# Optimization experiments

Hardware: AMD Instinct MI355X
Metric: run time of the kernel (lower is better)

## Reference

```python
import jax, jax.numpy as jnp
import numpy as np

N_NODES = 500_000
N_EDGES = 16_000_000


def setup_inputs() -> dict:
    key = jax.random.key(0)
    ks = jax.random.split(key, 8)
    x = jax.random.normal(ks[0], (N_NODES, 6), dtype=jnp.float32)
    edge_index = jax.random.randint(ks[1], (2, N_EDGES), 0, N_NODES, dtype=jnp.int64)
    conv_w = jax.random.normal(ks[2], (4, 6), dtype=jnp.float32) * 0.4
    conv_b = jax.random.normal(ks[3], (4,), dtype=jnp.float32) * 0.1
    fc1_w = jax.random.normal(ks[4], (64, 4), dtype=jnp.float32) * 0.5
    fc1_b = jax.random.normal(ks[5], (64,), dtype=jnp.float32) * 0.1
    fc3_w = jax.random.normal(ks[6], (10, 64), dtype=jnp.float32) * 0.125
    fc3_b = jax.random.normal(ks[7], (10,), dtype=jnp.float32) * 0.1
    return {"x": x, "edge_index": edge_index, "conv_w": conv_w, "conv_b": conv_b,
            "fc1_w": fc1_w, "fc1_b": fc1_b, "fc3_w": fc3_w, "fc3_b": fc3_b}


def reference(x, edge_index, conv_w, conv_b, fc1_w, fc1_b, fc3_w, fc3_b):
    n = x.shape[0]
    loop = jnp.arange(n, dtype=edge_index.dtype)
    # PyG GCNConv default: add self-loops, symmetric normalization
    row = jnp.concatenate([edge_index[0], loop])  # source
    col = jnp.concatenate([edge_index[1], loop])  # target (aggregation index)
    deg = jax.ops.segment_sum(jnp.ones_like(col, dtype=x.dtype), col, num_segments=n)
    dinv = jnp.where(deg > 0, deg ** -0.5, 0.0).astype(x.dtype)
    norm = dinv[row] * dinv[col]                  # [E+N]
    h = x @ conv_w.T                              # [N, 4]
    msg = h[row] * norm[:, None]                  # gather + scale
    agg = jax.ops.segment_sum(msg, col, num_segments=n) + conv_b  # scatter-add
    t = jnp.tanh(agg)
    # F.dropout treated as identity (deterministic eval reference)
    g = jnp.mean(t, axis=0, keepdims=True)        # global_mean_pool, batch=None -> [1, 4]
    hdn = jax.nn.relu(g @ fc1_w.T + fc1_b)
    out = hdn @ fc3_w.T + fc3_b                   # [1, output_size]
    return out
```

## Files before the change

kernel.cpp:

```cpp
#include <hip/hip_runtime.h>
#include <hip/hip_fp16.h>
#include <math.h>


constexpr int NP = 1024;
constexpr int SHIFT = 10;
constexpr unsigned MASK = 1023;
constexpr int NPART_MAX = 512;
constexpr int EPB = 8192;
constexpr int BINB = 512;
constexpr int BT = 512;
constexpr int SPLIT = 4;

struct alignas(8) Half4 { __half2 a, b; };

typedef unsigned u32x4 __attribute__((ext_vector_type(4)));
typedef int      i32x4 __attribute__((ext_vector_type(4)));
typedef float    f32x4 __attribute__((ext_vector_type(4)));


__global__ __launch_bounds__(BINB) void k_bin(const int* __restrict__ row,
                                              const int* __restrict__ col, int E,
                                              int P, int cap, int* __restrict__ cursor,
                                              unsigned* __restrict__ binned) {
    __shared__ unsigned lbuf[EPB];
    __shared__ int lcount[NPART_MAX];
    __shared__ int lbase[NPART_MAX];
    __shared__ int gbase[NPART_MAX];
    __shared__ int lpos[NPART_MAX];
    __shared__ int sc[NPART_MAX];

    int t = threadIdx.x;
    int start = blockIdx.x * EPB;
    int end = min(start + EPB, E);
    bool full = (end - start) == EPB;

    lcount[t] = 0; lpos[t] = 0;
    __syncthreads();

    if (full) {
        const int4* c4 = (const int4*)(col + start);
#pragma unroll
        for (int i = 0; i < EPB / 4 / BINB; ++i) {
            int4 c = c4[t + i * BINB];
            atomicAdd(&lcount[c.x >> SHIFT], 1);
            atomicAdd(&lcount[c.y >> SHIFT], 1);
            atomicAdd(&lcount[c.z >> SHIFT], 1);
            atomicAdd(&lcount[c.w >> SHIFT], 1);
        }
    } else {
        for (int e = start + t; e < end; e += BINB)
            atomicAdd(&lcount[col[e] >> SHIFT], 1);
    }
    __syncthreads();

    sc[t] = lcount[t];
    __syncthreads();
    for (int off = 1; off < NPART_MAX; off <<= 1) {
        int v = (t >= off) ? sc[t - off] : 0;
        __syncthreads();
        sc[t] += v;
        __syncthreads();
    }
    lbase[t] = sc[t] - lcount[t];
    if (t < P) {
        int c = lcount[t];
        gbase[t] = (c > 0) ? atomicAdd(&cursor[t], c) : 0;
    }
    __syncthreads();

    if (full) {
        const int4* c4 = (const int4*)(col + start);
        const i32x4* r4 = (const i32x4*)(row + start);
#pragma unroll
        for (int i = 0; i < EPB / 4 / BINB; ++i) {
            int4 c = c4[t + i * BINB];
            i32x4 r = __builtin_nontemporal_load(&r4[t + i * BINB]);
            int part, slot;
            part = c.x >> SHIFT; slot = atomicAdd(&lpos[part], 1);
            lbuf[lbase[part] + slot] = ((unsigned)r.x << SHIFT) | ((unsigned)c.x & MASK);
            part = c.y >> SHIFT; slot = atomicAdd(&lpos[part], 1);
            lbuf[lbase[part] + slot] = ((unsigned)r.y << SHIFT) | ((unsigned)c.y & MASK);
            part = c.z >> SHIFT; slot = atomicAdd(&lpos[part], 1);
            lbuf[lbase[part] + slot] = ((unsigned)r.z << SHIFT) | ((unsigned)c.z & MASK);
            part = c.w >> SHIFT; slot = atomicAdd(&lpos[part], 1);
            lbuf[lbase[part] + slot] = ((unsigned)r.w << SHIFT) | ((unsigned)c.w & MASK);
        }
    } else {
        for (int e = start + t; e < end; e += BINB) {
            int r = row[e], c = col[e];
            int part = c >> SHIFT;
            int slot = atomicAdd(&lpos[part], 1);
            lbuf[lbase[part] + slot] = ((unsigned)r << SHIFT) | ((unsigned)c & MASK);
        }
    }
    __syncthreads();

    int lane = t & 63;
    int wave = t >> 6;
    const int nwaves = BINB / 64;
    for (int part = wave; part < P; part += nwaves) {
        int cnt = lcount[part];
        if (cnt == 0) continue;
        int lb = lbase[part];
        int gb = gbase[part];
        unsigned* dst = binned + (size_t)part * cap;
        for (int j = lane; j < cnt; j += 64) {
            int slot = gb + j;
            if (slot < cap) __builtin_nontemporal_store(lbuf[lb + j], &dst[slot]);
        }
    }
}

__global__ __launch_bounds__(BT) void k_deg_bin(const unsigned* __restrict__ binned,
                                                const int* __restrict__ cursor, int cap,
                                                int n, int* __restrict__ deg) {
    __shared__ int degs[NP];
    int part = blockIdx.x / SPLIT;
    int sub = blockIdx.x - part * SPLIT;
    int tid = threadIdx.x;
    for (int i = tid; i < NP; i += BT) degs[i] = 0;
    __syncthreads();
    int cnt = min(cursor[part], cap);
    const unsigned* bin = binned + (size_t)part * cap;
    const u32x4* bin4 = (const u32x4*)bin;
    int cnt4 = cnt >> 2;
    for (int i = tid + sub * BT; i < cnt4; i += BT * SPLIT) {
        u32x4 v = __builtin_nontemporal_load(&bin4[i]);
        atomicAdd(&degs[v.x & MASK], 1);
        atomicAdd(&degs[v.y & MASK], 1);
        atomicAdd(&degs[v.z & MASK], 1);
        atomicAdd(&degs[v.w & MASK], 1);
    }
    if (sub == 0) {
        for (int e = (cnt4 << 2) + tid; e < cnt; e += BT)
            atomicAdd(&degs[bin[e] & MASK], 1);
    }
    __syncthreads();
    int base = part * NP;
    for (int i = tid; i < NP; i += BT) {
        int node = base + i;
        if (node < n && degs[i] > 0) atomicAdd(&deg[node], degs[i]);
    }
}

__global__ __launch_bounds__(256) void k_node2(const float* __restrict__ x,
                                               const float* __restrict__ conv_w,
                                               const int* __restrict__ deg, int n,
                                               Half4* __restrict__ ph,
                                               float* __restrict__ dinvg) {
    __shared__ float w[24];
    if (threadIdx.x < 24) w[threadIdx.x] = conv_w[threadIdx.x];
    __syncthreads();
    int i = blockIdx.x * 256 + threadIdx.x;
    if (i >= n) return;
    float dinv = rsqrtf((float)(deg[i] + 1));
    const float* xr = x + (size_t)i * 6;
    float2 a = *(const float2*)xr;
    float2 b = *(const float2*)(xr + 2);
    float2 cc = *(const float2*)(xr + 4);
    float xv[6] = {a.x, a.y, b.x, b.y, cc.x, cc.y};
    float h0 = 0.f, h1 = 0.f, h2 = 0.f, h3 = 0.f;
#pragma unroll
    for (int j = 0; j < 6; ++j) {
        h0 += xv[j] * w[j];
        h1 += xv[j] * w[6 + j];
        h2 += xv[j] * w[12 + j];
        h3 += xv[j] * w[18 + j];
    }
    Half4 o;
    o.a = __floats2half2_rn(h0 * dinv, h1 * dinv);
    o.b = __floats2half2_rn(h2 * dinv, h3 * dinv);
    ph[i] = o;
    dinvg[i] = dinv;
}

__global__ __launch_bounds__(BT) void k_acc(const unsigned* __restrict__ binned,
                                            const int* __restrict__ cursor, int cap,
                                            const Half4* __restrict__ ph,
                                            const float* __restrict__ dinvg,
                                            const float* __restrict__ conv_b, int n,
                                            float* __restrict__ gsum) {
    __shared__ float S[NP * 5];
    __shared__ float4 red[BT / 64];
    int part = blockIdx.x;
    int tid = threadIdx.x;
    for (int i = tid; i < NP * 5; i += BT) S[i] = 0.f;
    __syncthreads();
    int cnt = min(cursor[part], cap);
    const unsigned* bin = binned + (size_t)part * cap;
    const u32x4* bin4 = (const u32x4*)bin;
    int cnt4 = cnt >> 2;
    for (int i = tid; i < cnt4; i += BT) {
        u32x4 v = __builtin_nontemporal_load(&bin4[i]);
        Half4 h0 = ph[v.x >> SHIFT];
        Half4 h1 = ph[v.y >> SHIFT];
        Half4 h2 = ph[v.z >> SHIFT];
        Half4 h3 = ph[v.w >> SHIFT];
        float2 a, b; float* s;
        a = __half22float2(h0.a); b = __half22float2(h0.b); s = &S[(v.x & MASK) * 5];
        atomicAdd(s + 0, a.x); atomicAdd(s + 1, a.y); atomicAdd(s + 2, b.x); atomicAdd(s + 3, b.y);
        a = __half22float2(h1.a); b = __half22float2(h1.b); s = &S[(v.y & MASK) * 5];
        atomicAdd(s + 0, a.x); atomicAdd(s + 1, a.y); atomicAdd(s + 2, b.x); atomicAdd(s + 3, b.y);
        a = __half22float2(h2.a); b = __half22float2(h2.b); s = &S[(v.z & MASK) * 5];
        atomicAdd(s + 0, a.x); atomicAdd(s + 1, a.y); atomicAdd(s + 2, b.x); atomicAdd(s + 3, b.y);
        a = __half22float2(h3.a); b = __half22float2(h3.b); s = &S[(v.w & MASK) * 5];
        atomicAdd(s + 0, a.x); atomicAdd(s + 1, a.y); atomicAdd(s + 2, b.x); atomicAdd(s + 3, b.y);
    }
    for (int e = (cnt4 << 2) + tid; e < cnt; e += BT) {
        unsigned v = bin[e];
        Half4 h = ph[v >> SHIFT];
        float2 a = __half22float2(h.a), b = __half22float2(h.b);
        float* s = &S[(v & MASK) * 5];
        atomicAdd(s + 0, a.x); atomicAdd(s + 1, a.y); atomicAdd(s + 2, b.x); atomicAdd(s + 3, b.y);
    }
    __syncthreads();
    float b0 = conv_b[0], b1 = conv_b[1], b2 = conv_b[2], b3 = conv_b[3];
    float4 acc = {0.f, 0.f, 0.f, 0.f};
    int base = part * NP;
    for (int i = tid; i < NP; i += BT) {
        int node = base + i;
        if (node >= n) continue;
        float di = dinvg[node];
        Half4 hp = ph[node];
        float2 pa = __half22float2(hp.a), pb = __half22float2(hp.b);
        acc.x += tanhf(di * (S[i * 5 + 0] + pa.x) + b0);
        acc.y += tanhf(di * (S[i * 5 + 1] + pa.y) + b1);
        acc.z += tanhf(di * (S[i * 5 + 2] + pb.x) + b2);
        acc.w += tanhf(di * (S[i * 5 + 3] + pb.y) + b3);
    }
#pragma unroll
    for (int off = 32; off > 0; off >>= 1) {
        acc.x += __shfl_down(acc.x, off);
        acc.y += __shfl_down(acc.y, off);
        acc.z += __shfl_down(acc.z, off);
        acc.w += __shfl_down(acc.w, off);
    }
    int lane = tid & 63, wv = tid >> 6;
    if (lane == 0) red[wv] = acc;
    __syncthreads();
    if (tid == 0) {
        float4 tt = red[0];
        for (int k = 1; k < BT / 64; ++k) {
            tt.x += red[k].x; tt.y += red[k].y; tt.z += red[k].z; tt.w += red[k].w;
        }
        unsafeAtomicAdd(&gsum[0], tt.x);
        unsafeAtomicAdd(&gsum[1], tt.y);
        unsafeAtomicAdd(&gsum[2], tt.z);
        unsafeAtomicAdd(&gsum[3], tt.w);
    }
}

__global__ void k_head(const float* __restrict__ gsum,
                       const float* __restrict__ fc1w, const float* __restrict__ fc1b,
                       const float* __restrict__ fc3w, const float* __restrict__ fc3b,
                       float* __restrict__ out, int n) {
    __shared__ float hdn[64];
    int t = threadIdx.x;
    float g[4];
    float inv_n = 1.0f / (float)n;
#pragma unroll
    for (int j = 0; j < 4; ++j) g[j] = gsum[j] * inv_n;
    if (t < 64) {
        float a = fc1b[t];
#pragma unroll
        for (int j = 0; j < 4; ++j) a += g[j] * fc1w[t * 4 + j];
        hdn[t] = fmaxf(a, 0.f);
    }
    __syncthreads();
    if (t < 10) {
        float a = fc3b[t];
#pragma unroll
        for (int k = 0; k < 64; ++k) a += hdn[k] * fc3w[t * 64 + k];
        out[t] = a;
    }
}


__global__ void k_deg(const int* __restrict__ col, int n_edges, int* __restrict__ deg) {
    int t = blockIdx.x * blockDim.x + threadIdx.x;
    int base = t * 4;
    if (base + 4 <= n_edges) {
        int4 c = *(const int4*)(col + base);
        atomicAdd(&deg[c.x], 1); atomicAdd(&deg[c.y], 1);
        atomicAdd(&deg[c.z], 1); atomicAdd(&deg[c.w], 1);
    } else {
        for (int e = base; e < n_edges; ++e) atomicAdd(&deg[col[e]], 1);
    }
}

__global__ void k_node(const float* __restrict__ x, const float* __restrict__ conv_w,
                       const int* __restrict__ deg, float4* __restrict__ p, int n) {
    int i = blockIdx.x * blockDim.x + threadIdx.x;
    if (i >= n) return;
    const float* xr = x + (size_t)i * 6;
    float2 a = *(const float2*)xr;
    float2 b = *(const float2*)(xr + 2);
    float2 c = *(const float2*)(xr + 4);
    float xv[6] = {a.x, a.y, b.x, b.y, c.x, c.y};
    float dinv = rsqrtf((float)(deg[i] + 1));
    float h0 = 0.f, h1 = 0.f, h2 = 0.f, h3 = 0.f;
#pragma unroll
    for (int j = 0; j < 6; ++j) {
        h0 += xv[j] * conv_w[j];
        h1 += xv[j] * conv_w[6 + j];
        h2 += xv[j] * conv_w[12 + j];
        h3 += xv[j] * conv_w[18 + j];
    }
    float4 o; o.x = h0 * dinv; o.y = h1 * dinv; o.z = h2 * dinv; o.w = h3 * dinv;
    p[i] = o;
}

__global__ void k_scatter(const int* __restrict__ row, const int* __restrict__ col, int n_edges,
                          const float4* __restrict__ p, float* __restrict__ S) {
    int t = blockIdx.x * blockDim.x + threadIdx.x;
    int base = t * 2;
    if (base + 2 <= n_edges) {
        int2 r = *(const int2*)(row + base);
        int2 c = *(const int2*)(col + base);
        float4 p0 = p[r.x], p1 = p[r.y];
        float* s0 = S + 4 * c.x;
        unsafeAtomicAdd(s0 + 0, p0.x); unsafeAtomicAdd(s0 + 1, p0.y);
        unsafeAtomicAdd(s0 + 2, p0.z); unsafeAtomicAdd(s0 + 3, p0.w);
        float* s1 = S + 4 * c.y;
        unsafeAtomicAdd(s1 + 0, p1.x); unsafeAtomicAdd(s1 + 1, p1.y);
        unsafeAtomicAdd(s1 + 2, p1.z); unsafeAtomicAdd(s1 + 3, p1.w);
    } else {
        for (int e = base; e < n_edges; ++e) {
            int r = row[e], c = col[e];
            float4 pv = p[r];
            float* s = S + 4 * c;
            unsafeAtomicAdd(s + 0, pv.x); unsafeAtomicAdd(s + 1, pv.y);
            unsafeAtomicAdd(s + 2, pv.z); unsafeAtomicAdd(s + 3, pv.w);
        }
    }
}

__global__ void k_reduce(const float4* __restrict__ S4, const float4* __restrict__ p,
                         const int* __restrict__ deg, const float* __restrict__ conv_b,
                         int n, float* __restrict__ gsum) {
    int i = blockIdx.x * blockDim.x + threadIdx.x;
    float4 v = {0.f, 0.f, 0.f, 0.f};
    if (i < n) {
        float dinv = rsqrtf((float)(deg[i] + 1));
        float4 s = S4[i];
        float4 pp = p[i];
        v.x = tanhf(dinv * (s.x + pp.x) + conv_b[0]);
        v.y = tanhf(dinv * (s.y + pp.y) + conv_b[1]);
        v.z = tanhf(dinv * (s.z + pp.z) + conv_b[2]);
        v.w = tanhf(dinv * (s.w + pp.w) + conv_b[3]);
    }
#pragma unroll
    for (int off = 32; off > 0; off >>= 1) {
        v.x += __shfl_down(v.x, off);
        v.y += __shfl_down(v.y, off);
        v.z += __shfl_down(v.z, off);
        v.w += __shfl_down(v.w, off);
    }
    __shared__ float4 lds[4];
    int lane = threadIdx.x & 63, w = threadIdx.x >> 6;
    if (lane == 0) lds[w] = v;
    __syncthreads();
    if (threadIdx.x == 0) {
        float4 tt = lds[0];
        for (int k = 1; k < 4; ++k) {
            tt.x += lds[k].x; tt.y += lds[k].y; tt.z += lds[k].z; tt.w += lds[k].w;
        }
        unsafeAtomicAdd(&gsum[0], tt.x); unsafeAtomicAdd(&gsum[1], tt.y);
        unsafeAtomicAdd(&gsum[2], tt.z); unsafeAtomicAdd(&gsum[3], tt.w);
    }
}


extern "C" void kernel_launch(void* const* d_in, const int* in_sizes, int n_in,
                              void* d_out, int out_size, void* d_ws, size_t ws_size,
                              hipStream_t stream) {
    const float* x      = (const float*)d_in[0];
    const int*   ei     = (const int*)d_in[1];
    const float* conv_w = (const float*)d_in[2];
    const float* conv_b = (const float*)d_in[3];
    const float* fc1w   = (const float*)d_in[4];
    const float* fc1b   = (const float*)d_in[5];
    const float* fc3w   = (const float*)d_in[6];
    const float* fc3b   = (const float*)d_in[7];

    int n = in_sizes[0] / 6;
    int E = in_sizes[1] / 2;
    const int* row = ei;
    const int* col = ei + E;

    int P = (n + NP - 1) / NP;
    int avg = (E + P - 1) / P;
    int cap = ((avg + avg / 32 + 1024) + 15) & ~15;

    size_t off = 0;
    size_t cursor_off = off;          off += (size_t)P * sizeof(int);
    off = (off + 15) & ~(size_t)15;
    size_t gsum_off = off;            off += 4 * sizeof(float);
    off = (off + 15) & ~(size_t)15;
    size_t deg_off = off;             off += (size_t)n * sizeof(int);
    size_t zero_end = off;
    off = (off + 15) & ~(size_t)15;
    size_t dinv_off = off;            off += (size_t)n * sizeof(float);
    off = (off + 15) & ~(size_t)15;
    size_t ph_off = off;              off += (size_t)n * sizeof(Half4);
    off = (off + 15) & ~(size_t)15;
    size_t bin_off = off;             off += (size_t)P * cap * sizeof(unsigned);
    size_t need = off;

    char* ws = (char*)d_ws;
    bool use_bin = (ws_size >= need) && (P <= NPART_MAX) && (n < (1 << 21));

    if (use_bin) {
        int* cursor = (int*)(ws + cursor_off);
        float* gsum = (float*)(ws + gsum_off);
        int* deg = (int*)(ws + deg_off);
        float* dinvg = (float*)(ws + dinv_off);
        Half4* ph = (Half4*)(ws + ph_off);
        unsigned* binned = (unsigned*)(ws + bin_off);

        hipMemsetAsync(d_ws, 0, zero_end, stream);
        int bin_blocks = (E + EPB - 1) / EPB;
        k_bin<<<bin_blocks, BINB, 0, stream>>>(row, col, E, P, cap, cursor, binned);
        k_deg_bin<<<P * SPLIT, BT, 0, stream>>>(binned, cursor, cap, n, deg);
        k_node2<<<(n + 255) / 256, 256, 0, stream>>>(x, conv_w, deg, n, ph, dinvg);
        k_acc<<<P, BT, 0, stream>>>(binned, cursor, cap, ph, dinvg, conv_b, n, gsum);
        k_head<<<1, 64, 0, stream>>>(gsum, fc1w, fc1b, fc3w, fc3b, (float*)d_out, n);
    } else {
        size_t o = 0;
        int* deg = (int*)(ws + o);      o += (size_t)n * sizeof(int);
        o = (o + 15) & ~(size_t)15;
        float* S = (float*)(ws + o);    o += (size_t)n * 4 * sizeof(float);
        float* gsum = (float*)(ws + o);
        size_t zend = o + 4 * sizeof(float);
        o = (zend + 15) & ~(size_t)15;
        float4* p = (float4*)(ws + o);

        hipMemsetAsync(d_ws, 0, zend, stream);
        int t1 = (E + 3) / 4;
        k_deg<<<(t1 + 255) / 256, 256, 0, stream>>>(col, E, deg);
        k_node<<<(n + 255) / 256, 256, 0, stream>>>(x, conv_w, deg, p, n);
        int t3 = (E + 1) / 2;
        k_scatter<<<(t3 + 255) / 256, 256, 0, stream>>>(row, col, E, p, S);
        k_reduce<<<(n + 255) / 256, 256, 0, stream>>>((const float4*)S, p, deg, conv_b, n, gsum);
        k_head<<<1, 64, 0, stream>>>(gsum, fc1w, fc1b, fc3w, fc3b, (float*)d_out, n);
    }
}
```

Measured before the change: 645.2 us.

## Bin edges into 4096-node tiles, sub-sort by source chunk, use FP8 features

Adds a new primary path that bins edges into 4096-node destination tiles and then counting-sorts each tile's edges by 8192-node source chunk. The accumulate kernel can then stage each source chunk's packed features in LDS and do the gather from shared memory instead of random global reads. Node features are packed as FP8 in 4 bytes per node, halving gather bandwidth compared with the old half4 layout. The cost is an extra sort pass, an extra sorted buffer, a separate finish kernel, and a loss of precision from FP8.

```diff
diff --git a/kernel.cpp b/kernel.cpp
--- a/kernel.cpp
+++ b/kernel.cpp
@@ -2,14 +2,24 @@
 #include <hip/hip_fp16.h>
 #include <math.h>
 
+
+constexpr int EPB = 8192;
+constexpr int BINB = 512;
+constexpr int BT = 512;
+
+constexpr int DPS = 12;
+constexpr int DP = 1 << DPS;
+constexpr unsigned DMASK = DP - 1;
+constexpr int NT_MAX = 128;
+constexpr int CHS = 13;
+constexpr int CH = 1 << CHS;
+constexpr int NCH_MAX = 64;
+constexpr int SPAD = DP + 8;
 
 constexpr int NP = 1024;
 constexpr int SHIFT = 10;
 constexpr unsigned MASK = 1023;
 constexpr int NPART_MAX = 512;
-constexpr int EPB = 8192;
-constexpr int BINB = 512;
-constexpr int BT = 512;
 constexpr int SPLIT = 4;
 
 struct alignas(8) Half4 { __half2 a, b; };
@@ -17,12 +27,301 @@
 typedef unsigned u32x4 __attribute__((ext_vector_type(4)));
 typedef int      i32x4 __attribute__((ext_vector_type(4)));
 typedef float    f32x4 __attribute__((ext_vector_type(4)));
-
-
-__global__ __launch_bounds__(BINB) void k_bin(const int* __restrict__ row,
-                                              const int* __restrict__ col, int E,
-                                              int P, int cap, int* __restrict__ cursor,
-                                              unsigned* __restrict__ binned) {
+typedef float    f32x2 __attribute__((ext_vector_type(2)));
+
+
+__global__ __launch_bounds__(BINB) void k_bin12(const int* __restrict__ row,
+                                                const int* __restrict__ col, int E,
+                                                int NT, int cap, int* __restrict__ cursor,
+                                                unsigned* __restrict__ binned) {
+    __shared__ unsigned lbuf[EPB];
+    __shared__ int lcount[NT_MAX];
+    __shared__ int lbase[NT_MAX];
+    __shared__ int gbase[NT_MAX];
+    __shared__ int lpos[NT_MAX];
+    __shared__ int sc[NT_MAX];
+
+    int t = threadIdx.x;
+    int start = blockIdx.x * EPB;
+    int end = min(start + EPB, E);
+    bool full = (end - start) == EPB;
+
+    if (t < NT_MAX) { lcount[t] = 0; lpos[t] = 0; }
+    __syncthreads();
+
+    if (full) {
+        const int4* c4 = (const int4*)(col + start);
+#pragma unroll
+        for (int i = 0; i < EPB / 4 / BINB; ++i) {
+            int4 c = c4[t + i * BINB];
+            atomicAdd(&lcount[c.x >> DPS], 1);
+            atomicAdd(&lcount[c.y >> DPS], 1);
+            atomicAdd(&lcount[c.z >> DPS], 1);
+            atomicAdd(&lcount[c.w >> DPS], 1);
+        }
+    } else {
+        for (int e = start + t; e < end; e += BINB)
+            atomicAdd(&lcount[col[e] >> DPS], 1);
+    }
+    __syncthreads();
+
+    if (t < NT_MAX) sc[t] = lcount[t];
+    __syncthreads();
+    for (int off = 1; off < NT_MAX; off <<= 1) {
+        int v = (t >= off && t < NT_MAX) ? sc[t - off] : 0;
+        __syncthreads();
+        if (t < NT_MAX) sc[t] += v;
+        __syncthreads();
+    }
+    if (t < NT_MAX) lbase[t] = sc[t] - lcount[t];
+    if (t < NT) {
+        int c = lcount[t];
+        gbase[t] = (c > 0) ? atomicAdd(&cursor[t], c) : 0;
+    }
+    __syncthreads();
+
+    if (full) {
+        const int4* c4 = (const int4*)(col + start);
+        const i32x4* r4 = (const i32x4*)(row + start);
+#pragma unroll
+        for (int i = 0; i < EPB / 4 / BINB; ++i) {
+            int4 c = c4[t + i * BINB];
+            i32x4 r = __builtin_nontemporal_load(&r4[t + i * BINB]);
+            int tile, slot;
+            tile = c.x >> DPS; slot = atomicAdd(&lpos[tile], 1);
+            lbuf[lbase[tile] + slot] = ((unsigned)r.x << DPS) | ((unsigned)c.x & DMASK);
+            tile = c.y >> DPS; slot = atomicAdd(&lpos[tile], 1);
+            lbuf[lbase[tile] + slot] = ((unsigned)r.y << DPS) | ((unsigned)c.y & DMASK);
+            tile = c.z >> DPS; slot = atomicAdd(&lpos[tile], 1);
+            lbuf[lbase[tile] + slot] = ((unsigned)r.z << DPS) | ((unsigned)c.z & DMASK);
+            tile = c.w >> DPS; slot = atomicAdd(&lpos[tile], 1);
+            lbuf[lbase[tile] + slot] = ((unsigned)r.w << DPS) | ((unsigned)c.w & DMASK);
+        }
+    } else {
+        for (int e = start + t; e < end; e += BINB) {
+            int r = row[e], c = col[e];
+            int tile = c >> DPS;
+            int slot = atomicAdd(&lpos[tile], 1);
+            lbuf[lbase[tile] + slot] = ((unsigned)r << DPS) | ((unsigned)c & DMASK);
+        }
+    }
+    __syncthreads();
+
+    int lane = t & 63;
+    int wave = t >> 6;
+    const int nwaves = BINB / 64;
+    for (int tile = wave; tile < NT; tile += nwaves) {
+        int cnt = lcount[tile];
+        if (cnt == 0) continue;
+        int lb = lbase[tile];
+        int gb = gbase[tile];
+        unsigned* dst = binned + (size_t)tile * cap;
+        for (int j = lane; j < cnt; j += 64) {
+            int slot = gb + j;
+            if (slot < cap) __builtin_nontemporal_store(lbuf[lb + j], &dst[slot]);
+        }
+    }
+}
+
+__global__ __launch_bounds__(BT) void k_sort(const unsigned* __restrict__ binned,
+                                             const int* __restrict__ cursor, int cap,
+                                             int n, int nch, int* __restrict__ deg,
+                                             unsigned* __restrict__ sorted,
+                                             int* __restrict__ dir) {
+    __shared__ int hist[NCH_MAX];
+    __shared__ int cur[NCH_MAX];
+    __shared__ int degs[DP];
+    int part = blockIdx.x >> 1;
+    int sub = blockIdx.x & 1;
+    int tid = threadIdx.x;
+    if (tid < NCH_MAX) hist[tid] = 0;
+    for (int i = tid; i < DP; i += BT) degs[i] = 0;
+    __syncthreads();
+
+    int cnt = min(cursor[part], cap);
+    int half = cnt >> 1;
+    int start = sub ? half : 0;
+    int endd = sub ? cnt : half;
+    const unsigned* bin = binned + (size_t)part * cap;
+
+    for (int i = start + tid; i < endd; i += BT) {
+        unsigned v = bin[i];
+        atomicAdd(&hist[v >> 25], 1);
+        atomicAdd(&degs[v & DMASK], 1);
+    }
+    __syncthreads();
+
+    if (tid == 0) {
+        int* dd = dir + (part * 2 + sub) * (nch + 1);
+        int run = 0;
+        for (int c = 0; c < nch; ++c) {
+            dd[c] = run;
+            cur[c] = run;
+            run += hist[c];
+        }
+        dd[nch] = run;
+    }
+    __syncthreads();
+
+    unsigned* out = sorted + (size_t)part * cap + (size_t)sub * (cap >> 1);
+    for (int i = start + tid; i < endd; i += BT) {
+        unsigned v = bin[i];
+        int c = v >> 25;
+        int slot = atomicAdd(&cur[c], 1);
+        out[slot] = (((v >> DPS) & (CH - 1)) << DPS) | (v & DMASK);
+    }
+
+    int base = part * DP;
+    for (int i = tid; i < DP; i += BT) {
+        int node = base + i;
+        if (node < n && degs[i] > 0) atomicAdd(&deg[node], degs[i]);
+    }
+}
+
+__global__ __launch_bounds__(256) void k_node8(const float* __restrict__ x,
+                                               const float* __restrict__ conv_w,
+                                               const int* __restrict__ deg, int n,
+                                               unsigned* __restrict__ ph) {
+    __shared__ float w[24];
+    if (threadIdx.x < 24) w[threadIdx.x] = conv_w[threadIdx.x];
+    __syncthreads();
+    int i = blockIdx.x * 256 + threadIdx.x;
+    if (i >= n) return;
+    float dinv = rsqrtf((float)(deg[i] + 1));
+    const float* xr = x + (size_t)i * 6;
+    float2 a = *(const float2*)xr;
+    float2 b = *(const float2*)(xr + 2);
+    float2 cc = *(const float2*)(xr + 4);
+    float xv[6] = {a.x, a.y, b.x, b.y, cc.x, cc.y};
+    float h0 = 0.f, h1 = 0.f, h2 = 0.f, h3 = 0.f;
+#pragma unroll
+    for (int j = 0; j < 6; ++j) {
+        h0 += xv[j] * w[j];
+        h1 += xv[j] * w[6 + j];
+        h2 += xv[j] * w[12 + j];
+        h3 += xv[j] * w[18 + j];
+    }
+    int pk = 0;
+    pk = __builtin_amdgcn_cvt_pk_fp8_f32(h0 * dinv, h1 * dinv, pk, false);
+    pk = __builtin_amdgcn_cvt_pk_fp8_f32(h2 * dinv, h3 * dinv, pk, true);
+    ph[i] = (unsigned)pk;
+}
+
+__global__ __launch_bounds__(BT) void k_acc4(const unsigned* __restrict__ sorted,
+                                             const int* __restrict__ dir, int cap,
+                                             const unsigned* __restrict__ ph,
+                                             int n, int nch,
+                                             float* __restrict__ Sg) {
+    __shared__ unsigned stage[CH];
+    __shared__ float S[4 * SPAD];
+    int part = blockIdx.x >> 1;
+    int sub = blockIdx.x & 1;
+    int tid = threadIdx.x;
+    for (int i = tid; i < 4 * SPAD; i += BT) S[i] = 0.f;
+
+    const unsigned* src = sorted + (size_t)part * cap + (size_t)sub * (cap >> 1);
+    const int* dd = dir + (part * 2 + sub) * (nch + 1);
+    __syncthreads();
+
+    for (int c = 0; c < nch; ++c) {
+        int cbase = c << CHS;
+        int lim = min(CH, n - cbase);
+        for (int i = tid; i < lim; i += BT) stage[i] = ph[cbase + i];
+        int s0 = dd[c], s1 = dd[c + 1];
+        __syncthreads();
+        for (int i = s0 + tid; i < s1; i += BT) {
+            unsigned w = src[i];
+            unsigned p = stage[w >> DPS];
+            unsigned d = w & DMASK;
+            f32x2 lo = __builtin_amdgcn_cvt_pk_f32_fp8((int)p, false);
+            f32x2 hi = __builtin_amdgcn_cvt_pk_f32_fp8((int)p, true);
+            atomicAdd(&S[d], lo.x);
+            atomicAdd(&S[SPAD + d], lo.y);
+            atomicAdd(&S[2 * SPAD + d], hi.x);
+            atomicAdd(&S[3 * SPAD + d], hi.y);
+        }
+        __syncthreads();
+    }
+
+    int base = part * DP;
+    for (int i = tid; i < DP * 4; i += BT) {
+        int node = base + (i >> 2);
+        if (node < n)
+            unsafeAtomicAdd(&Sg[(size_t)base * 4 + i], S[(i & 3) * SPAD + (i >> 2)]);
+    }
+}
+
+__global__ __launch_bounds__(256) void k_finish8(const float* __restrict__ Sg,
+                                                 const unsigned* __restrict__ ph,
+                                                 const int* __restrict__ deg,
+                                                 const float* __restrict__ conv_b, int n,
+                                                 float* __restrict__ gsum) {
+    int i = blockIdx.x * 256 + threadIdx.x;
+    float4 v = {0.f, 0.f, 0.f, 0.f};
+    if (i < n) {
+        float dinv = rsqrtf((float)(deg[i] + 1));
+        f32x4 s = __builtin_nontemporal_load((const f32x4*)Sg + i);
+        unsigned p = ph[i];
+        f32x2 lo = __builtin_amdgcn_cvt_pk_f32_fp8((int)p, false);
+        f32x2 hi = __builtin_amdgcn_cvt_pk_f32_fp8((int)p, true);
+        v.x = tanhf(dinv * (s.x + lo.x) + conv_b[0]);
+        v.y = tanhf(dinv * (s.y + lo.y) + conv_b[1]);
+        v.z = tanhf(dinv * (s.z + hi.x) + conv_b[2]);
+        v.w = tanhf(dinv * (s.w + hi.y) + conv_b[3]);
+    }
+#pragma unroll
+    for (int off = 32; off > 0; off >>= 1) {
+        v.x += __shfl_down(v.x, off);
+        v.y += __shfl_down(v.y, off);
+        v.z += __shfl_down(v.z, off);
+        v.w += __shfl_down(v.w, off);
+    }
+    __shared__ float4 red[4];
+    int lane = threadIdx.x & 63, w = threadIdx.x >> 6;
+    if (lane == 0) red[w] = v;
+    __syncthreads();
+    if (threadIdx.x == 0) {
+        float4 tt = red[0];
+        for (int k = 1; k < 4; ++k) {
+            tt.x += red[k].x; tt.y += red[k].y; tt.z += red[k].z; tt.w += red[k].w;
+        }
+        unsafeAtomicAdd(&gsum[0], tt.x);
+        unsafeAtomicAdd(&gsum[1], tt.y);
+        unsafeAtomicAdd(&gsum[2], tt.z);
+        unsafeAtomicAdd(&gsum[3], tt.w);
+    }
+}
+
+__global__ void k_head(const float* __restrict__ gsum,
+                       const float* __restrict__ fc1w, const float* __restrict__ fc1b,
+                       const float* __restrict__ fc3w, const float* __restrict__ fc3b,
+                       float* __restrict__ out, int n) {
+    __shared__ float hdn[64];
+    int t = threadIdx.x;
+    float g[4];
+    float inv_n = 1.0f / (float)n;
+#pragma unroll
+    for (int j = 0; j < 4; ++j) g[j] = gsum[j] * inv_n;
+    if (t < 64) {
+        float a = fc1b[t];
+#pragma unroll
+        for (int j = 0; j < 4; ++j) a += g[j] * fc1w[t * 4 + j];
+        hdn[t] = fmaxf(a, 0.f);
+    }
+    __syncthreads();
+    if (t < 10) {
+        float a = fc3b[t];
+#pragma unroll
+        for (int k = 0; k < 64; ++k) a += hdn[k] * fc3w[t * 64 + k];
+        out[t] = a;
+    }
+}
+
+
+__global__ __launch_bounds__(BINB) void k_bin10(const int* __restrict__ row,
+                                                const int* __restrict__ col, int E,
+                                                int P, int cap, int* __restrict__ cursor,
+                                                unsigned* __restrict__ binned) {
     __shared__ unsigned lbuf[EPB];
     __shared__ int lcount[NPART_MAX];
     __shared__ int lbase[NPART_MAX];
@@ -144,11 +443,11 @@
     }
 }
 
-__global__ __launch_bounds__(256) void k_node2(const float* __restrict__ x,
-                                               const float* __restrict__ conv_w,
-                                               const int* __restrict__ deg, int n,
-                                               Half4* __restrict__ ph,
-                                               float* __restrict__ dinvg) {
+__global__ __launch_bounds__(256) void k_node2h(const float* __restrict__ x,
+                                                const float* __restrict__ conv_w,
+                                                const int* __restrict__ deg, int n,
+                                                Half4* __restrict__ ph,
+                                                float* __restrict__ dinvg) {
     __shared__ float w[24];
     if (threadIdx.x < 24) w[threadIdx.x] = conv_w[threadIdx.x];
     __syncthreads();
@@ -248,31 +547,6 @@
         unsafeAtomicAdd(&gsum[1], tt.y);
         unsafeAtomicAdd(&gsum[2], tt.z);
         unsafeAtomicAdd(&gsum[3], tt.w);
-    }
-}
-
-__global__ void k_head(const float* __restrict__ gsum,
-                       const float* __restrict__ fc1w, const float* __restrict__ fc1b,
-                       const float* __restrict__ fc3w, const float* __restrict__ fc3b,
-                       float* __restrict__ out, int n) {
-    __shared__ float hdn[64];
-    int t = threadIdx.x;
-    float g[4];
-    float inv_n = 1.0f / (float)n;
-#pragma unroll
-    for (int j = 0; j < 4; ++j) g[j] = gsum[j] * inv_n;
-    if (t < 64) {
-        float a = fc1b[t];
-#pragma unroll
-        for (int j = 0; j < 4; ++j) a += g[j] * fc1w[t * 4 + j];
-        hdn[t] = fmaxf(a, 0.f);
-    }
-    __syncthreads();
-    if (t < 10) {
-        float a = fc3b[t];
-#pragma unroll
-        for (int k = 0; k < 64; ++k) a += hdn[k] * fc3w[t * 64 + k];
-        out[t] = a;
     }
 }
 
@@ -389,44 +663,94 @@
     const int* row = ei;
     const int* col = ei + E;
 
-    int P = (n + NP - 1) / NP;
-    int avg = (E + P - 1) / P;
-    int cap = ((avg + avg / 32 + 1024) + 15) & ~15;
-
-    size_t off = 0;
-    size_t cursor_off = off;          off += (size_t)P * sizeof(int);
-    off = (off + 15) & ~(size_t)15;
-    size_t gsum_off = off;            off += 4 * sizeof(float);
-    off = (off + 15) & ~(size_t)15;
-    size_t deg_off = off;             off += (size_t)n * sizeof(int);
-    size_t zero_end = off;
-    off = (off + 15) & ~(size_t)15;
-    size_t dinv_off = off;            off += (size_t)n * sizeof(float);
-    off = (off + 15) & ~(size_t)15;
-    size_t ph_off = off;              off += (size_t)n * sizeof(Half4);
-    off = (off + 15) & ~(size_t)15;
-    size_t bin_off = off;             off += (size_t)P * cap * sizeof(unsigned);
-    size_t need = off;
-
     char* ws = (char*)d_ws;
-    bool use_bin = (ws_size >= need) && (P <= NPART_MAX) && (n < (1 << 21));
-
-    if (use_bin) {
-        int* cursor = (int*)(ws + cursor_off);
-        float* gsum = (float*)(ws + gsum_off);
-        int* deg = (int*)(ws + deg_off);
-        float* dinvg = (float*)(ws + dinv_off);
-        Half4* ph = (Half4*)(ws + ph_off);
-        unsigned* binned = (unsigned*)(ws + bin_off);
-
-        hipMemsetAsync(d_ws, 0, zero_end, stream);
-        int bin_blocks = (E + EPB - 1) / EPB;
-        k_bin<<<bin_blocks, BINB, 0, stream>>>(row, col, E, P, cap, cursor, binned);
-        k_deg_bin<<<P * SPLIT, BT, 0, stream>>>(binned, cursor, cap, n, deg);
-        k_node2<<<(n + 255) / 256, 256, 0, stream>>>(x, conv_w, deg, n, ph, dinvg);
-        k_acc<<<P, BT, 0, stream>>>(binned, cursor, cap, ph, dinvg, conv_b, n, gsum);
-        k_head<<<1, 64, 0, stream>>>(gsum, fc1w, fc1b, fc3w, fc3b, (float*)d_out, n);
-    } else {
+
+    {
+        int PD = (n + DP - 1) / DP;
+        int nch = (n + CH - 1) >> CHS;
+        int avg = (E + PD - 1) / PD;
+        int cap = ((avg + avg / 64 + 3072) + 15) & ~15;
+
+        size_t off = 0;
+        size_t cursor_off = off;      off += (size_t)NT_MAX * sizeof(int);
+        size_t gsum_off = off;        off += 4 * sizeof(float);
+        off = (off + 15) & ~(size_t)15;
+        size_t deg_off = off;         off += (size_t)n * sizeof(int);
+        off = (off + 15) & ~(size_t)15;
+        size_t S_off = off;           off += (size_t)n * 4 * sizeof(float);
+        size_t zero_end = off;
+        off = (off + 15) & ~(size_t)15;
+        size_t ph_off = off;          off += (size_t)n * sizeof(unsigned);
+        off = (off + 15) & ~(size_t)15;
+        size_t bin_off = off;         off += (size_t)PD * cap * sizeof(unsigned);
+        off = (off + 15) & ~(size_t)15;
+        size_t sort_off = off;        off += (size_t)PD * cap * sizeof(unsigned);
+        off = (off + 15) & ~(size_t)15;
+        size_t dir_off = off;         off += (size_t)PD * 2 * (nch + 1) * sizeof(int);
+        size_t need1 = off;
+
+        if (ws_size >= need1 && n <= (1 << 19) && PD <= NT_MAX && nch <= NCH_MAX) {
+            int* cursor = (int*)(ws + cursor_off);
+            float* gsum = (float*)(ws + gsum_off);
+            int* deg = (int*)(ws + deg_off);
+            float* Sg = (float*)(ws + S_off);
+            unsigned* ph = (unsigned*)(ws + ph_off);
+            unsigned* binned = (unsigned*)(ws + bin_off);
+            unsigned* sorted = (unsigned*)(ws + sort_off);
+            int* dir = (int*)(ws + dir_off);
+
+            hipMemsetAsync(d_ws, 0, zero_end, stream);
+            int bin_blocks = (E + EPB - 1) / EPB;
+            k_bin12<<<bin_blocks, BINB, 0, stream>>>(row, col, E, PD, cap, cursor, binned);
+            k_sort<<<PD * 2, BT, 0, stream>>>(binned, cursor, cap, n, nch, deg, sorted, dir);
+            k_node8<<<(n + 255) / 256, 256, 0, stream>>>(x, conv_w, deg, n, ph);
+            k_acc4<<<PD * 2, BT, 0, stream>>>(sorted, dir, cap, ph, n, nch, Sg);
+            k_finish8<<<(n + 255) / 256, 256, 0, stream>>>(Sg, ph, deg, conv_b, n, gsum);
+            k_head<<<1, 64, 0, stream>>>(gsum, fc1w, fc1b, fc3w, fc3b, (float*)d_out, n);
+            return;
+        }
+    }
+
+    {
+        int P = (n + NP - 1) / NP;
+        int avg = (E + P - 1) / P;
+        int cap = ((avg + avg / 32 + 1024) + 15) & ~15;
+
+        size_t off = 0;
+        size_t cursor_off = off;      off += (size_t)P * sizeof(int);
+        off = (off + 15) & ~(size_t)15;
+        size_t gsum_off = off;        off += 4 * sizeof(float);
+        off = (off + 15) & ~(size_t)15;
+        size_t deg_off = off;         off += (size_t)n * sizeof(int);
+        size_t zero_end = off;
+        off = (off + 15) & ~(size_t)15;
+        size_t dinv_off = off;        off += (size_t)n * sizeof(float);
+        off = (off + 15) & ~(size_t)15;
+        size_t ph_off = off;          off += (size_t)n * sizeof(Half4);
+        off = (off + 15) & ~(size_t)15;
+        size_t bin_off = off;         off += (size_t)P * cap * sizeof(unsigned);
+        size_t need2 = off;
+
+        if (ws_size >= need2 && P <= NPART_MAX && n < (1 << 21)) {
+            int* cursor = (int*)(ws + cursor_off);
+            float* gsum = (float*)(ws + gsum_off);
+            int* deg = (int*)(ws + deg_off);
+            float* dinvg = (float*)(ws + dinv_off);
+            Half4* ph = (Half4*)(ws + ph_off);
+            unsigned* binned = (unsigned*)(ws + bin_off);
+
+            hipMemsetAsync(d_ws, 0, zero_end, stream);
+            int bin_blocks = (E + EPB - 1) / EPB;
+            k_bin10<<<bin_blocks, BINB, 0, stream>>>(row, col, E, P, cap, cursor, binned);
+            k_deg_bin<<<P * SPLIT, BT, 0, stream>>>(binned, cursor, cap, n, deg);
+            k_node2h<<<(n + 255) / 256, 256, 0, stream>>>(x, conv_w, deg, n, ph, dinvg);
+            k_acc<<<P, BT, 0, stream>>>(binned, cursor, cap, ph, dinvg, conv_b, n, gsum);
+            k_head<<<1, 64, 0, stream>>>(gsum, fc1w, fc1b, fc3w, fc3b, (float*)d_out, n);
+            return;
+        }
+    }
+
+    {
         size_t o = 0;
         int* deg = (int*)(ws + o);      o += (size_t)n * sizeof(int);
         o = (o + 15) & ~(size_t)15;
```

Measured after the change: 885.9 us. +37.3%, slower.
